# Optimization experiments

Measured on AMD Instinct MI355X. Metric: run time of the kernel, lower is better.

The kernel has to match this reference:

```python
import jax, jax.numpy as jnp
import numpy as np

ATTN_MULT = 8.0
NEG_INF = float('-inf')

N, Q, S, D = 16, 2048, 2048, 64


def setup_inputs() -> dict:
    key = jax.random.key(0)
    kq, kk, kv, kp = jax.random.split(key, 4)
    return {
        "queries_nqd": jax.random.normal(kq, (N, Q, D), dtype=jnp.float32),
        "keys_nsd": jax.random.normal(kk, (N, S, D), dtype=jnp.float32),
        "values_nsv": jax.random.normal(kv, (N, S, D), dtype=jnp.float32),
        "prefix_len_n": jax.random.randint(kp, (N,), 0, S, dtype=jnp.int64 if jax.config.jax_enable_x64 else jnp.int32),
    }


def reference(queries_nqd, keys_nsd, values_nsv, prefix_len_n):
    # attention_type == 'block_diagonal', backend == 'torch', dropout p == 0
    n, q, d = queries_nqd.shape
    s = keys_nsd.shape[1]
    scale = ATTN_MULT / d
    # prefix-block mask: key position < prefix_len (broadcast over queries)
    block_mask_n1s = (jnp.arange(s)[None, None, :] < prefix_len_n[:, None, None])  # [n,1,s]
    diag_mask_qs = jnp.arange(q)[:, None] == jnp.arange(s)[None, :]                # [q,s]
    mask_nqs = block_mask_n1s | diag_mask_qs[None, :, :]                           # [n,q,s]
    scores_nqs = jnp.einsum('nqd,nsd->nqs', queries_nqd, keys_nsd) * scale
    scores_nqs = jnp.where(mask_nqs, scores_nqs, NEG_INF)
    probs_nqs = jax.nn.softmax(scores_nqs, axis=-1)
    return jnp.einsum('nqs,nsv->nqv', probs_nqs, values_nsv)
```

## Files before the change

### kernel.cpp

```cpp
#include <hip/hip_runtime.h>
#include <hip/hip_bf16.h>
#include <math.h>

#define NH 16
#define QL 2048
#define SL 2048
#define DD 64
#define BQ 128
#define NSPLIT 2
#define PSTR 72
#define QK_SCALE_LOG2E 0.1803368801111f

typedef __attribute__((ext_vector_type(8))) short short8;
typedef __attribute__((ext_vector_type(4))) float floatx4;
typedef __attribute__((ext_vector_type(4))) unsigned short ushort4v;
typedef __attribute__((ext_vector_type(8))) unsigned short ushort8v;

__device__ __forceinline__ unsigned short f2bf(float x) {
    unsigned u = __float_as_uint(x);
    u += 0x7FFFu + ((u >> 16) & 1u);
    return (unsigned short)(u >> 16);
}
__device__ __forceinline__ unsigned int f2bf2u(float x, float y) {
    __hip_bfloat162 h = __float22bfloat162_rn(make_float2(x, y));
    return *(unsigned int*)&h;
}
__device__ __forceinline__ float bf2f(unsigned short h) {
    return __uint_as_float((unsigned)h << 16);
}

__device__ __forceinline__ void gld16(const unsigned short* g, unsigned short* l) {
    __builtin_amdgcn_global_load_lds(
        (const __attribute__((address_space(1))) unsigned int*)g,
        (__attribute__((address_space(3))) unsigned int*)l, 16, 0, 0);
}

__global__ __launch_bounds__(512) void k_prep(
    const float* __restrict__ Kf, const float* __restrict__ Vf,
    unsigned short* __restrict__ Kb, unsigned short* __restrict__ Vtb)
{
    __shared__ unsigned short sT[64][PSTR];
    const int bx = (int)blockIdx.x, tid = (int)threadIdx.x;

    const int gidx = bx * 512 + tid;
    #pragma unroll
    for (int k = 0; k < 2; ++k) {
        int idx = gidx + k * (512 * 512);
        float4 v = ((const float4*)Kf)[idx];
        ushort4v h = { f2bf(v.x), f2bf(v.y), f2bf(v.z), f2bf(v.w) };
        *(ushort4v*)(Kb + (size_t)idx * 4) = h;
    }

    const int n = bx >> 5, s0 = (bx & 31) * 64;
    const float* vb = Vf + ((size_t)n * SL + s0) * DD;
    #pragma unroll
    for (int i = 0; i < 2; ++i) {
        int idx = tid + i * 512;
        int r = idx >> 4, c = (idx & 15) << 2;
        float4 v = *(const float4*)(vb + r * DD + c);
        sT[c + 0][r] = f2bf(v.x);
        sT[c + 1][r] = f2bf(v.y);
        sT[c + 2][r] = f2bf(v.z);
        sT[c + 3][r] = f2bf(v.w);
    }
    __syncthreads();
    const int d = tid >> 3, sg = tid & 7;
    unsigned short* out = Vtb + (size_t)n * DD * SL + (size_t)d * SL + s0 + sg * 8;
    ushort8v a;
    #pragma unroll
    for (int i = 0; i < 8; ++i) a[i] = sT[d][sg * 8 + i];
    *(ushort8v*)out = a;
}

__global__ __launch_bounds__(512, 4) void k_attn(
    const float* __restrict__ Qf, const unsigned short* __restrict__ Kb,
    const unsigned short* __restrict__ Vtb, const int* __restrict__ plen_g,
    unsigned short* __restrict__ Opb, float* __restrict__ Lp)
{
    __shared__ unsigned short sK[3][64 * 64];
    __shared__ unsigned short sVt[3][64 * 64];
    __shared__ unsigned short sP[8 * 16 * 64];

    const int flat = (int)blockIdx.x;
    const int sp   = flat >> 8;
    const int rb   = flat & 255;
    const int n    = (rb + sp) & (NH - 1);
    const int qt   = rb >> 4;
    const int q0   = qt * BQ;
    const int plen = plen_g[n];

    const int tid  = (int)threadIdx.x;
    const int wave = tid >> 6, lane = tid & 63, quad = lane >> 4, l16 = lane & 15;

    const int ptiles = (plen + 63) >> 6;
    const int d0     = q0 >> 6;
    const int tdiag  = d0 + sp;
    const int cnt_p  = (ptiles + 1 - sp) >> 1;
    const int total  = cnt_p + (tdiag >= ptiles ? 1 : 0);

    const int qrow  = wave * 16 + l16;
    const int qglob = q0 + qrow;
    const int pmask = (l16 & 7) * 8;

    const unsigned short* kh = Kb  + (size_t)n * SL * DD;
    const unsigned short* vh = Vtb + (size_t)n * DD * SL;

    const int srow = wave * 8 + (lane >> 3);
    const int scol = ((lane & 7) ^ (srow & 7)) * 8;

    auto tile_of = [&](int i) -> int {
        return (i < cnt_p) ? (sp + (i << 1)) : tdiag;
    };
    auto stage = [&](int t, int b) {
        const unsigned short* kg = kh + ((size_t)t << 6) * DD;
        const unsigned short* vg = vh + (t << 6);
        gld16(kg + srow * DD + scol, sK[b] + wave * 512);
        gld16(vg + (size_t)srow * SL + scol, sVt[b] + wave * 512);
    };

    short8 bQ0, bQ1;
    {
        const float* qf = Qf + ((size_t)(n * QL + qglob)) * DD + quad * 8;
        float4 a0 = *(const float4*)(qf);
        float4 a1 = *(const float4*)(qf + 4);
        float4 c0 = *(const float4*)(qf + 32);
        float4 c1 = *(const float4*)(qf + 36);
        const float S = QK_SCALE_LOG2E;
        unsigned int u0[4] = {
            f2bf2u(a0.x * S, a0.y * S), f2bf2u(a0.z * S, a0.w * S),
            f2bf2u(a1.x * S, a1.y * S), f2bf2u(a1.z * S, a1.w * S) };
        unsigned int u1[4] = {
            f2bf2u(c0.x * S, c0.y * S), f2bf2u(c0.z * S, c0.w * S),
            f2bf2u(c1.x * S, c1.y * S), f2bf2u(c1.z * S, c1.w * S) };
        bQ0 = *(short8*)u0;
        bQ1 = *(short8*)u1;
    }

    stage(tile_of(0), 0);
    if (total > 1) stage(tile_of(1), 1);

    floatx4 acc[4];
    #pragma unroll
    for (int dt = 0; dt < 4; ++dt) acc[dt] = (floatx4){0.f, 0.f, 0.f, 0.f};
    float lsum = 0.f;
    unsigned short* pw = sP + qrow * 64;

    int bi = 0;
    int bs = 2;
    for (int i = 0; i < total; ++i) {
        if (i + 2 <= total) {
            asm volatile("s_waitcnt vmcnt(2) lgkmcnt(0)" ::: "memory");
        } else {
            asm volatile("s_waitcnt vmcnt(0) lgkmcnt(0)" ::: "memory");
        }
        __builtin_amdgcn_s_barrier();

        if (i + 2 < total) stage(tile_of(i + 2), bs);

        const unsigned short* sk = sK[bi];
        const unsigned short* sv = sVt[bi];
        const int t  = tile_of(i);
        const int s0 = t << 6;

        floatx4 sf[4];
        #pragma unroll
        for (int st2 = 0; st2 < 4; ++st2) sf[st2] = (floatx4){0.f, 0.f, 0.f, 0.f};
        __builtin_amdgcn_s_setprio(1);
        #pragma unroll
        for (int st2 = 0; st2 < 4; ++st2) {
            int krow = st2 * 16 + l16;
            short8 aK0 = *(const short8*)(sk + krow * 64 + (((0 * 4 + quad) ^ (krow & 7)) * 8));
            short8 aK1 = *(const short8*)(sk + krow * 64 + (((1 * 4 + quad) ^ (krow & 7)) * 8));
            sf[st2] = __builtin_amdgcn_mfma_f32_16x16x32_bf16(aK0, bQ0, sf[st2], 0, 0, 0);
            sf[st2] = __builtin_amdgcn_mfma_f32_16x16x32_bf16(aK1, bQ1, sf[st2], 0, 0, 0);
        }
        __builtin_amdgcn_s_setprio(0);

        if (s0 + 64 <= plen) {
            #pragma unroll
            for (int st2 = 0; st2 < 4; ++st2) {
                float p0 = __builtin_amdgcn_exp2f(sf[st2][0]);
                float p1 = __builtin_amdgcn_exp2f(sf[st2][1]);
                float p2 = __builtin_amdgcn_exp2f(sf[st2][2]);
                float p3 = __builtin_amdgcn_exp2f(sf[st2][3]);
                lsum += (p0 + p1) + (p2 + p3);
                uint2 pk = { f2bf2u(p0, p1), f2bf2u(p2, p3) };
                *(uint2*)(pw + ((st2 * 16 + quad * 4) ^ pmask)) = pk;
            }
        } else {
            #pragma unroll
            for (int st2 = 0; st2 < 4; ++st2) {
                float p[4];
                #pragma unroll
                for (int r2 = 0; r2 < 4; ++r2) {
                    int s = s0 + st2 * 16 + quad * 4 + r2;
                    bool valid = (s < plen) || (s == qglob);
                    p[r2] = __builtin_amdgcn_exp2f(valid ? sf[st2][r2] : -INFINITY);
                    lsum += p[r2];
                }
                uint2 pk = { f2bf2u(p[0], p[1]), f2bf2u(p[2], p[3]) };
                *(uint2*)(pw + ((st2 * 16 + quad * 4) ^ pmask)) = pk;
            }
        }

        __builtin_amdgcn_s_setprio(1);
        #pragma unroll
        for (int ks = 0; ks < 2; ++ks) {
            short8 aP = *(const short8*)(pw + ((ks * 32 + quad * 8) ^ pmask));
            #pragma unroll
            for (int dt = 0; dt < 4; ++dt) {
                int vrow = dt * 16 + l16;
                short8 bV = *(const short8*)(sv + vrow * 64 + (((ks * 4 + quad) ^ (vrow & 7)) * 8));
                acc[dt] = __builtin_amdgcn_mfma_f32_16x16x32_bf16(aP, bV, acc[dt], 0, 0, 0);
            }
        }
        __builtin_amdgcn_s_setprio(0);

        bi = (bi == 2) ? 0 : bi + 1;
        bs = (bs == 2) ? 0 : bs + 1;
    }

    lsum += __shfl_xor(lsum, 16, 64);
    lsum += __shfl_xor(lsum, 32, 64);
    if (quad == 0)
        Lp[((size_t)sp * NH + n) * QL + q0 + qrow] = lsum;

    unsigned short* pws = sP + wave * 16 * 64;
    #pragma unroll
    for (int dt = 0; dt < 4; ++dt) {
        int chunk = dt * 2 + (l16 >> 3);
        #pragma unroll
        for (int r2 = 0; r2 < 4; ++r2) {
            int row = quad * 4 + r2;
            int sw = ((chunk ^ (row & 7)) * 8) + (l16 & 7);
            pws[row * 64 + sw] = f2bf(acc[dt][r2]);
        }
    }
    const size_t qbase = ((size_t)sp * NH + n) * QL + q0 + wave * 16;
    #pragma unroll
    for (int t2 = 0; t2 < 2; ++t2) {
        int row = t2 * 8 + (lane >> 3);
        int chunk = lane & 7;
        int sw = (chunk ^ (row & 7)) * 8;
        ushort8v val = *(const ushort8v*)(pws + row * 64 + sw);
        *(ushort8v*)(Opb + (qbase + row) * DD + chunk * 8) = val;
    }
}

__global__ __launch_bounds__(512) void k_combine(
    const unsigned short* __restrict__ Opb, const float* __restrict__ Lp,
    float* __restrict__ Og)
{
    const int idx = (int)(blockIdx.x * 512 + threadIdx.x);
    const int d8 = idx & 7;
    const int q  = (idx >> 3) & (QL - 1);
    const int n  = idx >> 14;
    float s[8];
    #pragma unroll
    for (int j = 0; j < 8; ++j) s[j] = 0.f;
    float l = 0.f;
    #pragma unroll
    for (int sp = 0; sp < NSPLIT; ++sp) {
        const unsigned short* ob = Opb + (((size_t)sp * NH + n) * QL + q) * DD + d8 * 8;
        ushort8v v = *(const ushort8v*)ob;
        #pragma unroll
        for (int j = 0; j < 8; ++j) s[j] += bf2f(v[j]);
        l += Lp[((size_t)sp * NH + n) * QL + q];
    }
    const float inv = 1.0f / l;
    float4 o0 = { s[0] * inv, s[1] * inv, s[2] * inv, s[3] * inv };
    float4 o1 = { s[4] * inv, s[5] * inv, s[6] * inv, s[7] * inv };
    float* og = Og + ((size_t)n * QL + q) * DD + d8 * 8;
    *(float4*)og = o0;
    *(float4*)(og + 4) = o1;
}

extern "C" void kernel_launch(void* const* d_in, const int* in_sizes, int n_in,
                              void* d_out, int out_size, void* d_ws, size_t ws_size,
                              hipStream_t stream) {
    const float* Qf   = (const float*)d_in[0];
    const float* Kf   = (const float*)d_in[1];
    const float* Vf   = (const float*)d_in[2];
    const int*   plen = (const int*)d_in[3];
    float* Og = (float*)d_out;

    char* ws = (char*)d_ws;
    unsigned short* Kb  = (unsigned short*)(ws);
    unsigned short* Vtb = (unsigned short*)(ws + (4u << 20));
    unsigned short* Opb = (unsigned short*)(ws + (8u << 20));
    float*          Lp  = (float*)(ws + (16u << 20));

    k_prep<<<512, 512, 0, stream>>>(Kf, Vf, Kb, Vtb);
    k_attn<<<NSPLIT * 256, 512, 0, stream>>>(Qf, Kb, Vtb, plen, Opb, Lp);
    k_combine<<<512, 512, 0, stream>>>(Opb, Lp, Og);
}
```

Measured before the change: 104.4 us.

## Fuse split-KV combine into attention kernel using two wave groups per block

The two KV splits, previously separate blocks, now run as two 512-thread groups inside one 1024-thread block that share a block barrier. The partial outputs and row sums are merged through shared memory and the normalized fp32 result is written directly. This removes the combine kernel launch and the global round trip of bf16 partials and row sums. In exchange it doubles the shared memory per block. Both groups must loop to the larger tile count because they share a barrier, and the block size limits how many blocks fit per CU.

```diff
diff --git a/kernel.cpp b/kernel.cpp
--- a/kernel.cpp
+++ b/kernel.cpp
@@ -7,7 +7,6 @@
 #define SL 2048
 #define DD 64
 #define BQ 128
-#define NSPLIT 2
 #define PSTR 72
 #define QK_SCALE_LOG2E 0.1803368801111f
 
@@ -72,31 +71,35 @@
     *(ushort8v*)out = a;
 }
 
-__global__ __launch_bounds__(512, 4) void k_attn(
+__global__ __launch_bounds__(1024, 4) void k_attn(
     const float* __restrict__ Qf, const unsigned short* __restrict__ Kb,
     const unsigned short* __restrict__ Vtb, const int* __restrict__ plen_g,
-    unsigned short* __restrict__ Opb, float* __restrict__ Lp)
+    float* __restrict__ Og)
 {
-    __shared__ unsigned short sK[3][64 * 64];
-    __shared__ unsigned short sVt[3][64 * 64];
-    __shared__ unsigned short sP[8 * 16 * 64];
-
-    const int flat = (int)blockIdx.x;
-    const int sp   = flat >> 8;
-    const int rb   = flat & 255;
-    const int n    = (rb + sp) & (NH - 1);
-    const int qt   = rb >> 4;
+    __shared__ unsigned short sK[2][3][64 * 64];
+    __shared__ unsigned short sVt[2][3][64 * 64];
+    __shared__ unsigned short sP[2][8 * 16 * 64];
+    __shared__ float lsh[2][128];
+
+    const int bx   = (int)blockIdx.x;
+    const int n    = bx >> 4;
+    const int qt   = bx & 15;
     const int q0   = qt * BQ;
     const int plen = plen_g[n];
 
     const int tid  = (int)threadIdx.x;
-    const int wave = tid >> 6, lane = tid & 63, quad = lane >> 4, l16 = lane & 15;
+    const int g    = tid >> 9;
+    const int wave = (tid >> 6) & 7;
+    const int lane = tid & 63, quad = lane >> 4, l16 = lane & 15;
 
     const int ptiles = (plen + 63) >> 6;
     const int d0     = q0 >> 6;
-    const int tdiag  = d0 + sp;
-    const int cnt_p  = (ptiles + 1 - sp) >> 1;
-    const int total  = cnt_p + (tdiag >= ptiles ? 1 : 0);
+    const int tot0   = ((ptiles + 1) >> 1) + (d0 >= ptiles ? 1 : 0);
+    const int tot1   = (ptiles >> 1) + (d0 + 1 >= ptiles ? 1 : 0);
+    const int mtotal = (tot0 > tot1) ? tot0 : tot1;
+    const int cnt_p  = g ? (ptiles >> 1) : ((ptiles + 1) >> 1);
+    const int total  = g ? tot1 : tot0;
+    const int tdiag  = d0 + g;
 
     const int qrow  = wave * 16 + l16;
     const int qglob = q0 + qrow;
@@ -109,13 +112,13 @@
     const int scol = ((lane & 7) ^ (srow & 7)) * 8;
 
     auto tile_of = [&](int i) -> int {
-        return (i < cnt_p) ? (sp + (i << 1)) : tdiag;
+        return (i < cnt_p) ? (g + (i << 1)) : tdiag;
     };
     auto stage = [&](int t, int b) {
         const unsigned short* kg = kh + ((size_t)t << 6) * DD;
         const unsigned short* vg = vh + (t << 6);
-        gld16(kg + srow * DD + scol, sK[b] + wave * 512);
-        gld16(vg + (size_t)srow * SL + scol, sVt[b] + wave * 512);
+        gld16(kg + srow * DD + scol, sK[g][b] + wave * 512);
+        gld16(vg + (size_t)srow * SL + scol, sVt[g][b] + wave * 512);
     };
 
     short8 bQ0, bQ1;
@@ -143,78 +146,83 @@
     #pragma unroll
     for (int dt = 0; dt < 4; ++dt) acc[dt] = (floatx4){0.f, 0.f, 0.f, 0.f};
     float lsum = 0.f;
-    unsigned short* pw = sP + qrow * 64;
+    unsigned short* pw = sP[g] + qrow * 64;
 
     int bi = 0;
     int bs = 2;
-    for (int i = 0; i < total; ++i) {
-        if (i + 2 <= total) {
-            asm volatile("s_waitcnt vmcnt(2) lgkmcnt(0)" ::: "memory");
-        } else {
-            asm volatile("s_waitcnt vmcnt(0) lgkmcnt(0)" ::: "memory");
+    for (int i = 0; i < mtotal; ++i) {
+        if (i < total) {
+            if (i + 2 <= total) {
+                asm volatile("s_waitcnt vmcnt(2) lgkmcnt(0)" ::: "memory");
+            } else {
+                asm volatile("s_waitcnt vmcnt(0) lgkmcnt(0)" ::: "memory");
+            }
         }
         __builtin_amdgcn_s_barrier();
-
-        if (i + 2 < total) stage(tile_of(i + 2), bs);
-
-        const unsigned short* sk = sK[bi];
-        const unsigned short* sv = sVt[bi];
-        const int t  = tile_of(i);
-        const int s0 = t << 6;
-
-        floatx4 sf[4];
-        #pragma unroll
-        for (int st2 = 0; st2 < 4; ++st2) sf[st2] = (floatx4){0.f, 0.f, 0.f, 0.f};
-        __builtin_amdgcn_s_setprio(1);
-        #pragma unroll
-        for (int st2 = 0; st2 < 4; ++st2) {
-            int krow = st2 * 16 + l16;
-            short8 aK0 = *(const short8*)(sk + krow * 64 + (((0 * 4 + quad) ^ (krow & 7)) * 8));
-            short8 aK1 = *(const short8*)(sk + krow * 64 + (((1 * 4 + quad) ^ (krow & 7)) * 8));
-            sf[st2] = __builtin_amdgcn_mfma_f32_16x16x32_bf16(aK0, bQ0, sf[st2], 0, 0, 0);
-            sf[st2] = __builtin_amdgcn_mfma_f32_16x16x32_bf16(aK1, bQ1, sf[st2], 0, 0, 0);
-        }
-        __builtin_amdgcn_s_setprio(0);
-
-        if (s0 + 64 <= plen) {
+        __builtin_amdgcn_sched_barrier(0);
+
+        if (i < total) {
+            if (i + 2 < total) stage(tile_of(i + 2), bs);
+
+            const unsigned short* sk = sK[g][bi];
+            const unsigned short* sv = sVt[g][bi];
+            const int t  = tile_of(i);
+            const int s0 = t << 6;
+
+            floatx4 sf[4];
+            #pragma unroll
+            for (int st2 = 0; st2 < 4; ++st2) sf[st2] = (floatx4){0.f, 0.f, 0.f, 0.f};
+            __builtin_amdgcn_s_setprio(1);
             #pragma unroll
             for (int st2 = 0; st2 < 4; ++st2) {
-                float p0 = __builtin_amdgcn_exp2f(sf[st2][0]);
-                float p1 = __builtin_amdgcn_exp2f(sf[st2][1]);
-                float p2 = __builtin_amdgcn_exp2f(sf[st2][2]);
-                float p3 = __builtin_amdgcn_exp2f(sf[st2][3]);
-                lsum += (p0 + p1) + (p2 + p3);
-                uint2 pk = { f2bf2u(p0, p1), f2bf2u(p2, p3) };
-                *(uint2*)(pw + ((st2 * 16 + quad * 4) ^ pmask)) = pk;
-            }
-        } else {
-            #pragma unroll
-            for (int st2 = 0; st2 < 4; ++st2) {
-                float p[4];
+                int krow = st2 * 16 + l16;
+                short8 aK0 = *(const short8*)(sk + krow * 64 + (((0 * 4 + quad) ^ (krow & 7)) * 8));
+                short8 aK1 = *(const short8*)(sk + krow * 64 + (((1 * 4 + quad) ^ (krow & 7)) * 8));
+                sf[st2] = __builtin_amdgcn_mfma_f32_16x16x32_bf16(aK0, bQ0, sf[st2], 0, 0, 0);
+                sf[st2] = __builtin_amdgcn_mfma_f32_16x16x32_bf16(aK1, bQ1, sf[st2], 0, 0, 0);
+            }
+            __builtin_amdgcn_s_setprio(0);
+
+            if (s0 + 64 <= plen) {
                 #pragma unroll
-                for (int r2 = 0; r2 < 4; ++r2) {
-                    int s = s0 + st2 * 16 + quad * 4 + r2;
-                    bool valid = (s < plen) || (s == qglob);
-                    p[r2] = __builtin_amdgcn_exp2f(valid ? sf[st2][r2] : -INFINITY);
-                    lsum += p[r2];
+                for (int st2 = 0; st2 < 4; ++st2) {
+                    float p0 = __builtin_amdgcn_exp2f(sf[st2][0]);
+                    float p1 = __builtin_amdgcn_exp2f(sf[st2][1]);
+                    float p2 = __builtin_amdgcn_exp2f(sf[st2][2]);
+                    float p3 = __builtin_amdgcn_exp2f(sf[st2][3]);
+                    lsum += (p0 + p1) + (p2 + p3);
+                    uint2 pk = { f2bf2u(p0, p1), f2bf2u(p2, p3) };
+                    *(uint2*)(pw + ((st2 * 16 + quad * 4) ^ pmask)) = pk;
                 }
-                uint2 pk = { f2bf2u(p[0], p[1]), f2bf2u(p[2], p[3]) };
-                *(uint2*)(pw + ((st2 * 16 + quad * 4) ^ pmask)) = pk;
-            }
-        }
-
-        __builtin_amdgcn_s_setprio(1);
-        #pragma unroll
-        for (int ks = 0; ks < 2; ++ks) {
-            short8 aP = *(const short8*)(pw + ((ks * 32 + quad * 8) ^ pmask));
-            #pragma unroll
-            for (int dt = 0; dt < 4; ++dt) {
-                int vrow = dt * 16 + l16;
-                short8 bV = *(const short8*)(sv + vrow * 64 + (((ks * 4 + quad) ^ (vrow & 7)) * 8));
-                acc[dt] = __builtin_amdgcn_mfma_f32_16x16x32_bf16(aP, bV, acc[dt], 0, 0, 0);
-            }
-        }
-        __builtin_amdgcn_s_setprio(0);
+            } else {
+                #pragma unroll
+                for (int st2 = 0; st2 < 4; ++st2) {
+                    float p[4];
+                    #pragma unroll
+                    for (int r2 = 0; r2 < 4; ++r2) {
+                        int s = s0 + st2 * 16 + quad * 4 + r2;
+                        bool valid = (s < plen) || (s == qglob);
+                        p[r2] = __builtin_amdgcn_exp2f(valid ? sf[st2][r2] : -INFINITY);
+                        lsum += p[r2];
+                    }
+                    uint2 pk = { f2bf2u(p[0], p[1]), f2bf2u(p[2], p[3]) };
+                    *(uint2*)(pw + ((st2 * 16 + quad * 4) ^ pmask)) = pk;
+                }
+            }
+
+            __builtin_amdgcn_s_setprio(1);
+            #pragma unroll
+            for (int ks = 0; ks < 2; ++ks) {
+                short8 aP = *(const short8*)(pw + ((ks * 32 + quad * 8) ^ pmask));
+                #pragma unroll
+                for (int dt = 0; dt < 4; ++dt) {
+                    int vrow = dt * 16 + l16;
+                    short8 bV = *(const short8*)(sv + vrow * 64 + (((ks * 4 + quad) ^ (vrow & 7)) * 8));
+                    acc[dt] = __builtin_amdgcn_mfma_f32_16x16x32_bf16(aP, bV, acc[dt], 0, 0, 0);
+                }
+            }
+            __builtin_amdgcn_s_setprio(0);
+        }
 
         bi = (bi == 2) ? 0 : bi + 1;
         bs = (bs == 2) ? 0 : bs + 1;
@@ -223,56 +231,45 @@
     lsum += __shfl_xor(lsum, 16, 64);
     lsum += __shfl_xor(lsum, 32, 64);
     if (quad == 0)
-        Lp[((size_t)sp * NH + n) * QL + q0 + qrow] = lsum;
-
-    unsigned short* pws = sP + wave * 16 * 64;
-    #pragma unroll
-    for (int dt = 0; dt < 4; ++dt) {
-        int chunk = dt * 2 + (l16 >> 3);
+        lsh[g][wave * 16 + l16] = lsum;
+
+    if (g == 1) {
+        unsigned short* pws = sP[1] + wave * 16 * 64;
+        #pragma unroll
+        for (int dt = 0; dt < 4; ++dt) {
+            int chunk = dt * 2 + (l16 >> 3);
+            #pragma unroll
+            for (int r2 = 0; r2 < 4; ++r2) {
+                int row = quad * 4 + r2;
+                int sw = ((chunk ^ (row & 7)) * 8) + (l16 & 7);
+                pws[row * 64 + sw] = f2bf(acc[dt][r2]);
+            }
+        }
+    }
+    __syncthreads();
+
+    if (g == 0) {
+        const unsigned short* pws = sP[1] + wave * 16 * 64;
+        float inv[4];
         #pragma unroll
         for (int r2 = 0; r2 < 4; ++r2) {
             int row = quad * 4 + r2;
-            int sw = ((chunk ^ (row & 7)) * 8) + (l16 & 7);
-            pws[row * 64 + sw] = f2bf(acc[dt][r2]);
-        }
-    }
-    const size_t qbase = ((size_t)sp * NH + n) * QL + q0 + wave * 16;
-    #pragma unroll
-    for (int t2 = 0; t2 < 2; ++t2) {
-        int row = t2 * 8 + (lane >> 3);
-        int chunk = lane & 7;
-        int sw = (chunk ^ (row & 7)) * 8;
-        ushort8v val = *(const ushort8v*)(pws + row * 64 + sw);
-        *(ushort8v*)(Opb + (qbase + row) * DD + chunk * 8) = val;
-    }
-}
-
-__global__ __launch_bounds__(512) void k_combine(
-    const unsigned short* __restrict__ Opb, const float* __restrict__ Lp,
-    float* __restrict__ Og)
-{
-    const int idx = (int)(blockIdx.x * 512 + threadIdx.x);
-    const int d8 = idx & 7;
-    const int q  = (idx >> 3) & (QL - 1);
-    const int n  = idx >> 14;
-    float s[8];
-    #pragma unroll
-    for (int j = 0; j < 8; ++j) s[j] = 0.f;
-    float l = 0.f;
-    #pragma unroll
-    for (int sp = 0; sp < NSPLIT; ++sp) {
-        const unsigned short* ob = Opb + (((size_t)sp * NH + n) * QL + q) * DD + d8 * 8;
-        ushort8v v = *(const ushort8v*)ob;
+            float lt = lsh[0][wave * 16 + row] + lsh[1][wave * 16 + row];
+            inv[r2] = 1.0f / lt;
+        }
+        float* ob = Og + ((size_t)n * QL + q0 + wave * 16) * DD;
         #pragma unroll
-        for (int j = 0; j < 8; ++j) s[j] += bf2f(v[j]);
-        l += Lp[((size_t)sp * NH + n) * QL + q];
-    }
-    const float inv = 1.0f / l;
-    float4 o0 = { s[0] * inv, s[1] * inv, s[2] * inv, s[3] * inv };
-    float4 o1 = { s[4] * inv, s[5] * inv, s[6] * inv, s[7] * inv };
-    float* og = Og + ((size_t)n * QL + q) * DD + d8 * 8;
-    *(float4*)og = o0;
-    *(float4*)(og + 4) = o1;
+        for (int dt = 0; dt < 4; ++dt) {
+            int chunk = dt * 2 + (l16 >> 3);
+            #pragma unroll
+            for (int r2 = 0; r2 < 4; ++r2) {
+                int row = quad * 4 + r2;
+                int sw = ((chunk ^ (row & 7)) * 8) + (l16 & 7);
+                float o = (acc[dt][r2] + bf2f(pws[row * 64 + sw])) * inv[r2];
+                ob[row * DD + dt * 16 + l16] = o;
+            }
+        }
+    }
 }
 
 extern "C" void kernel_launch(void* const* d_in, const int* in_sizes, int n_in,
@@ -287,10 +284,7 @@
     char* ws = (char*)d_ws;
     unsigned short* Kb  = (unsigned short*)(ws);
     unsigned short* Vtb = (unsigned short*)(ws + (4u << 20));
-    unsigned short* Opb = (unsigned short*)(ws + (8u << 20));
-    float*          Lp  = (float*)(ws + (16u << 20));
 
     k_prep<<<512, 512, 0, stream>>>(Kf, Vf, Kb, Vtb);
-    k_attn<<<NSPLIT * 256, 512, 0, stream>>>(Qf, Kb, Vtb, plen, Opb, Lp);
-    k_combine<<<512, 512, 0, stream>>>(Opb, Lp, Og);
-}
+    k_attn<<<NH * (QL / BQ), 1024, 0, stream>>>(Qf, Kb, Vtb, plen, Og);
+}
```

New measurement: 106.1 us. About the same (+1.7%).

## Process two query halves per block to reuse K/V tiles, split keys four ways

Applied to the files above, without the earlier changes.

Each attention block now covers 256 query rows as two 128-row halves sharing every staged K and V^T tile, so the LDS loads and global staging are amortised over twice the MFMA work. To keep the grid at 512 blocks, the key dimension is split four ways instead of two, which doubles the partial-output traffic read by the combine kernel. Q is converted and pre-scaled to bf16 in the prep kernel rather than inside the attention kernel. The doubled accumulators and score registers raise register pressure under the existing launch bound, which risks spills or lower occupancy.

```diff
diff --git a/kernel.cpp b/kernel.cpp
--- a/kernel.cpp
+++ b/kernel.cpp
@@ -6,8 +6,8 @@
 #define QL 2048
 #define SL 2048
 #define DD 64
-#define BQ 128
-#define NSPLIT 2
+#define BQ 256
+#define NSPLIT 4
 #define PSTR 72
 #define QK_SCALE_LOG2E 0.1803368801111f
 
@@ -36,19 +36,27 @@
 }
 
 __global__ __launch_bounds__(512) void k_prep(
-    const float* __restrict__ Kf, const float* __restrict__ Vf,
-    unsigned short* __restrict__ Kb, unsigned short* __restrict__ Vtb)
+    const float* __restrict__ Qf, const float* __restrict__ Kf, const float* __restrict__ Vf,
+    unsigned short* __restrict__ Qb, unsigned short* __restrict__ Kb, unsigned short* __restrict__ Vtb)
 {
     __shared__ unsigned short sT[64][PSTR];
     const int bx = (int)blockIdx.x, tid = (int)threadIdx.x;
-
     const int gidx = bx * 512 + tid;
+
     #pragma unroll
     for (int k = 0; k < 2; ++k) {
         int idx = gidx + k * (512 * 512);
         float4 v = ((const float4*)Kf)[idx];
         ushort4v h = { f2bf(v.x), f2bf(v.y), f2bf(v.z), f2bf(v.w) };
         *(ushort4v*)(Kb + (size_t)idx * 4) = h;
+    }
+    #pragma unroll
+    for (int k = 0; k < 2; ++k) {
+        int idx = gidx + k * (512 * 512);
+        float4 v = ((const float4*)Qf)[idx];
+        const float S = QK_SCALE_LOG2E;
+        ushort4v h = { f2bf(v.x * S), f2bf(v.y * S), f2bf(v.z * S), f2bf(v.w * S) };
+        *(ushort4v*)(Qb + (size_t)idx * 4) = h;
     }
 
     const int n = bx >> 5, s0 = (bx & 31) * 64;
@@ -73,17 +81,17 @@
 }
 
 __global__ __launch_bounds__(512, 4) void k_attn(
-    const float* __restrict__ Qf, const unsigned short* __restrict__ Kb,
+    const unsigned short* __restrict__ Qb, const unsigned short* __restrict__ Kb,
     const unsigned short* __restrict__ Vtb, const int* __restrict__ plen_g,
     unsigned short* __restrict__ Opb, float* __restrict__ Lp)
 {
     __shared__ unsigned short sK[3][64 * 64];
     __shared__ unsigned short sVt[3][64 * 64];
-    __shared__ unsigned short sP[8 * 16 * 64];
+    __shared__ unsigned short sP[2][8 * 16 * 64];
 
     const int flat = (int)blockIdx.x;
-    const int sp   = flat >> 8;
-    const int rb   = flat & 255;
+    const int sp   = flat >> 7;
+    const int rb   = flat & 127;
     const int n    = (rb + sp) & (NH - 1);
     const int qt   = rb >> 4;
     const int q0   = qt * BQ;
@@ -95,11 +103,12 @@
     const int ptiles = (plen + 63) >> 6;
     const int d0     = q0 >> 6;
     const int tdiag  = d0 + sp;
-    const int cnt_p  = (ptiles + 1 - sp) >> 1;
+    const int cnt_p  = (ptiles + 3 - sp) >> 2;
     const int total  = cnt_p + (tdiag >= ptiles ? 1 : 0);
 
     const int qrow  = wave * 16 + l16;
-    const int qglob = q0 + qrow;
+    const int qgA   = q0 + qrow;
+    const int qgB   = qgA + 128;
     const int pmask = (l16 & 7) * 8;
 
     const unsigned short* kh = Kb  + (size_t)n * SL * DD;
@@ -109,7 +118,7 @@
     const int scol = ((lane & 7) ^ (srow & 7)) * 8;
 
     auto tile_of = [&](int i) -> int {
-        return (i < cnt_p) ? (sp + (i << 1)) : tdiag;
+        return (i < cnt_p) ? (sp + (i << 2)) : tdiag;
     };
     auto stage = [&](int t, int b) {
         const unsigned short* kg = kh + ((size_t)t << 6) * DD;
@@ -118,32 +127,25 @@
         gld16(vg + (size_t)srow * SL + scol, sVt[b] + wave * 512);
     };
 
-    short8 bQ0, bQ1;
-    {
-        const float* qf = Qf + ((size_t)(n * QL + qglob)) * DD + quad * 8;
-        float4 a0 = *(const float4*)(qf);
-        float4 a1 = *(const float4*)(qf + 4);
-        float4 c0 = *(const float4*)(qf + 32);
-        float4 c1 = *(const float4*)(qf + 36);
-        const float S = QK_SCALE_LOG2E;
-        unsigned int u0[4] = {
-            f2bf2u(a0.x * S, a0.y * S), f2bf2u(a0.z * S, a0.w * S),
-            f2bf2u(a1.x * S, a1.y * S), f2bf2u(a1.z * S, a1.w * S) };
-        unsigned int u1[4] = {
-            f2bf2u(c0.x * S, c0.y * S), f2bf2u(c0.z * S, c0.w * S),
-            f2bf2u(c1.x * S, c1.y * S), f2bf2u(c1.z * S, c1.w * S) };
-        bQ0 = *(short8*)u0;
-        bQ1 = *(short8*)u1;
-    }
+    const unsigned short* qbA = Qb + ((size_t)n * QL + qgA) * DD;
+    const unsigned short* qbB = qbA + 128 * DD;
+    short8 bQ0A = *(const short8*)(qbA + quad * 8);
+    short8 bQ1A = *(const short8*)(qbA + 32 + quad * 8);
+    short8 bQ0B = *(const short8*)(qbB + quad * 8);
+    short8 bQ1B = *(const short8*)(qbB + 32 + quad * 8);
 
     stage(tile_of(0), 0);
     if (total > 1) stage(tile_of(1), 1);
 
-    floatx4 acc[4];
-    #pragma unroll
-    for (int dt = 0; dt < 4; ++dt) acc[dt] = (floatx4){0.f, 0.f, 0.f, 0.f};
-    float lsum = 0.f;
-    unsigned short* pw = sP + qrow * 64;
+    floatx4 accA[4], accB[4];
+    #pragma unroll
+    for (int dt = 0; dt < 4; ++dt) {
+        accA[dt] = (floatx4){0.f, 0.f, 0.f, 0.f};
+        accB[dt] = (floatx4){0.f, 0.f, 0.f, 0.f};
+    }
+    float lsumA = 0.f, lsumB = 0.f;
+    unsigned short* pwA = sP[0] + qrow * 64;
+    unsigned short* pwB = sP[1] + qrow * 64;
 
     int bi = 0;
     int bs = 2;
@@ -162,56 +164,75 @@
         const int t  = tile_of(i);
         const int s0 = t << 6;
 
-        floatx4 sf[4];
-        #pragma unroll
-        for (int st2 = 0; st2 < 4; ++st2) sf[st2] = (floatx4){0.f, 0.f, 0.f, 0.f};
+        floatx4 sfA[4], sfB[4];
+        #pragma unroll
+        for (int st2 = 0; st2 < 4; ++st2) {
+            sfA[st2] = (floatx4){0.f, 0.f, 0.f, 0.f};
+            sfB[st2] = (floatx4){0.f, 0.f, 0.f, 0.f};
+        }
         __builtin_amdgcn_s_setprio(1);
         #pragma unroll
         for (int st2 = 0; st2 < 4; ++st2) {
             int krow = st2 * 16 + l16;
             short8 aK0 = *(const short8*)(sk + krow * 64 + (((0 * 4 + quad) ^ (krow & 7)) * 8));
             short8 aK1 = *(const short8*)(sk + krow * 64 + (((1 * 4 + quad) ^ (krow & 7)) * 8));
-            sf[st2] = __builtin_amdgcn_mfma_f32_16x16x32_bf16(aK0, bQ0, sf[st2], 0, 0, 0);
-            sf[st2] = __builtin_amdgcn_mfma_f32_16x16x32_bf16(aK1, bQ1, sf[st2], 0, 0, 0);
+            sfA[st2] = __builtin_amdgcn_mfma_f32_16x16x32_bf16(aK0, bQ0A, sfA[st2], 0, 0, 0);
+            sfA[st2] = __builtin_amdgcn_mfma_f32_16x16x32_bf16(aK1, bQ1A, sfA[st2], 0, 0, 0);
+            sfB[st2] = __builtin_amdgcn_mfma_f32_16x16x32_bf16(aK0, bQ0B, sfB[st2], 0, 0, 0);
+            sfB[st2] = __builtin_amdgcn_mfma_f32_16x16x32_bf16(aK1, bQ1B, sfB[st2], 0, 0, 0);
         }
         __builtin_amdgcn_s_setprio(0);
 
         if (s0 + 64 <= plen) {
             #pragma unroll
             for (int st2 = 0; st2 < 4; ++st2) {
-                float p0 = __builtin_amdgcn_exp2f(sf[st2][0]);
-                float p1 = __builtin_amdgcn_exp2f(sf[st2][1]);
-                float p2 = __builtin_amdgcn_exp2f(sf[st2][2]);
-                float p3 = __builtin_amdgcn_exp2f(sf[st2][3]);
-                lsum += (p0 + p1) + (p2 + p3);
-                uint2 pk = { f2bf2u(p0, p1), f2bf2u(p2, p3) };
-                *(uint2*)(pw + ((st2 * 16 + quad * 4) ^ pmask)) = pk;
+                float a0 = __builtin_amdgcn_exp2f(sfA[st2][0]);
+                float a1 = __builtin_amdgcn_exp2f(sfA[st2][1]);
+                float a2 = __builtin_amdgcn_exp2f(sfA[st2][2]);
+                float a3 = __builtin_amdgcn_exp2f(sfA[st2][3]);
+                lsumA += (a0 + a1) + (a2 + a3);
+                uint2 pkA = { f2bf2u(a0, a1), f2bf2u(a2, a3) };
+                *(uint2*)(pwA + ((st2 * 16 + quad * 4) ^ pmask)) = pkA;
+                float b0 = __builtin_amdgcn_exp2f(sfB[st2][0]);
+                float b1 = __builtin_amdgcn_exp2f(sfB[st2][1]);
+                float b2 = __builtin_amdgcn_exp2f(sfB[st2][2]);
+                float b3 = __builtin_amdgcn_exp2f(sfB[st2][3]);
+                lsumB += (b0 + b1) + (b2 + b3);
+                uint2 pkB = { f2bf2u(b0, b1), f2bf2u(b2, b3) };
+                *(uint2*)(pwB + ((st2 * 16 + quad * 4) ^ pmask)) = pkB;
             }
         } else {
             #pragma unroll
             for (int st2 = 0; st2 < 4; ++st2) {
-                float p[4];
+                float pa[4], pb[4];
                 #pragma unroll
                 for (int r2 = 0; r2 < 4; ++r2) {
                     int s = s0 + st2 * 16 + quad * 4 + r2;
-                    bool valid = (s < plen) || (s == qglob);
-                    p[r2] = __builtin_amdgcn_exp2f(valid ? sf[st2][r2] : -INFINITY);
-                    lsum += p[r2];
+                    bool va = (s < plen) || (s == qgA);
+                    bool vb = (s < plen) || (s == qgB);
+                    pa[r2] = __builtin_amdgcn_exp2f(va ? sfA[st2][r2] : -INFINITY);
+                    pb[r2] = __builtin_amdgcn_exp2f(vb ? sfB[st2][r2] : -INFINITY);
+                    lsumA += pa[r2];
+                    lsumB += pb[r2];
                 }
-                uint2 pk = { f2bf2u(p[0], p[1]), f2bf2u(p[2], p[3]) };
-                *(uint2*)(pw + ((st2 * 16 + quad * 4) ^ pmask)) = pk;
+                uint2 pkA = { f2bf2u(pa[0], pa[1]), f2bf2u(pa[2], pa[3]) };
+                uint2 pkB = { f2bf2u(pb[0], pb[1]), f2bf2u(pb[2], pb[3]) };
+                *(uint2*)(pwA + ((st2 * 16 + quad * 4) ^ pmask)) = pkA;
+                *(uint2*)(pwB + ((st2 * 16 + quad * 4) ^ pmask)) = pkB;
             }
         }
 
         __builtin_amdgcn_s_setprio(1);
         #pragma unroll
         for (int ks = 0; ks < 2; ++ks) {
-            short8 aP = *(const short8*)(pw + ((ks * 32 + quad * 8) ^ pmask));
+            short8 aPA = *(const short8*)(pwA + ((ks * 32 + quad * 8) ^ pmask));
+            short8 aPB = *(const short8*)(pwB + ((ks * 32 + quad * 8) ^ pmask));
             #pragma unroll
             for (int dt = 0; dt < 4; ++dt) {
                 int vrow = dt * 16 + l16;
                 short8 bV = *(const short8*)(sv + vrow * 64 + (((ks * 4 + quad) ^ (vrow & 7)) * 8));
-                acc[dt] = __builtin_amdgcn_mfma_f32_16x16x32_bf16(aP, bV, acc[dt], 0, 0, 0);
+                accA[dt] = __builtin_amdgcn_mfma_f32_16x16x32_bf16(aPA, bV, accA[dt], 0, 0, 0);
+                accB[dt] = __builtin_amdgcn_mfma_f32_16x16x32_bf16(aPB, bV, accB[dt], 0, 0, 0);
             }
         }
         __builtin_amdgcn_s_setprio(0);
@@ -220,12 +241,17 @@
         bs = (bs == 2) ? 0 : bs + 1;
     }
 
-    lsum += __shfl_xor(lsum, 16, 64);
-    lsum += __shfl_xor(lsum, 32, 64);
-    if (quad == 0)
-        Lp[((size_t)sp * NH + n) * QL + q0 + qrow] = lsum;
-
-    unsigned short* pws = sP + wave * 16 * 64;
+    lsumA += __shfl_xor(lsumA, 16, 64);
+    lsumA += __shfl_xor(lsumA, 32, 64);
+    lsumB += __shfl_xor(lsumB, 16, 64);
+    lsumB += __shfl_xor(lsumB, 32, 64);
+    if (quad == 0) {
+        Lp[((size_t)sp * NH + n) * QL + qgA] = lsumA;
+        Lp[((size_t)sp * NH + n) * QL + qgB] = lsumB;
+    }
+
+    unsigned short* pwsA = sP[0] + wave * 16 * 64;
+    unsigned short* pwsB = sP[1] + wave * 16 * 64;
     #pragma unroll
     for (int dt = 0; dt < 4; ++dt) {
         int chunk = dt * 2 + (l16 >> 3);
@@ -233,17 +259,21 @@
         for (int r2 = 0; r2 < 4; ++r2) {
             int row = quad * 4 + r2;
             int sw = ((chunk ^ (row & 7)) * 8) + (l16 & 7);
-            pws[row * 64 + sw] = f2bf(acc[dt][r2]);
-        }
-    }
-    const size_t qbase = ((size_t)sp * NH + n) * QL + q0 + wave * 16;
+            pwsA[row * 64 + sw] = f2bf(accA[dt][r2]);
+            pwsB[row * 64 + sw] = f2bf(accB[dt][r2]);
+        }
+    }
+    const size_t qbaseA = ((size_t)sp * NH + n) * QL + q0 + wave * 16;
+    const size_t qbaseB = qbaseA + 128;
     #pragma unroll
     for (int t2 = 0; t2 < 2; ++t2) {
         int row = t2 * 8 + (lane >> 3);
         int chunk = lane & 7;
         int sw = (chunk ^ (row & 7)) * 8;
-        ushort8v val = *(const ushort8v*)(pws + row * 64 + sw);
-        *(ushort8v*)(Opb + (qbase + row) * DD + chunk * 8) = val;
+        ushort8v valA = *(const ushort8v*)(pwsA + row * 64 + sw);
+        ushort8v valB = *(const ushort8v*)(pwsB + row * 64 + sw);
+        *(ushort8v*)(Opb + (qbaseA + row) * DD + chunk * 8) = valA;
+        *(ushort8v*)(Opb + (qbaseB + row) * DD + chunk * 8) = valB;
     }
 }
 
@@ -287,10 +317,11 @@
     char* ws = (char*)d_ws;
     unsigned short* Kb  = (unsigned short*)(ws);
     unsigned short* Vtb = (unsigned short*)(ws + (4u << 20));
-    unsigned short* Opb = (unsigned short*)(ws + (8u << 20));
-    float*          Lp  = (float*)(ws + (16u << 20));
-
-    k_prep<<<512, 512, 0, stream>>>(Kf, Vf, Kb, Vtb);
-    k_attn<<<NSPLIT * 256, 512, 0, stream>>>(Qf, Kb, Vtb, plen, Opb, Lp);
+    unsigned short* Qb  = (unsigned short*)(ws + (8u << 20));
+    unsigned short* Opb = (unsigned short*)(ws + (12u << 20));
+    float*          Lp  = (float*)(ws + (28u << 20));
+
+    k_prep<<<512, 512, 0, stream>>>(Qf, Kf, Vf, Qb, Kb, Vtb);
+    k_attn<<<NSPLIT * 128, 512, 0, stream>>>(Qb, Kb, Vtb, plen, Opb, Lp);
     k_combine<<<512, 512, 0, stream>>>(Opb, Lp, Og);
 }
```

Result: slower. 117.3 us (+12.4%).

## Fuse split-KV combine into attention kernel via last-block atomic counter

Applied to the files above, without the earlier changes.

Removes the separate combine kernel launch. Each attention block bumps a per-(head, q-tile) atomic counter after writing its partial output, and the last of the two splits reduces both partials into the final fp32 output. The counter is zeroed in the prep kernel. This saves one kernel launch and its scheduling gap, at the cost of a threadfence, an atomic per block, and tail work on the last-arriving block.

```diff
diff --git a/kernel.cpp b/kernel.cpp
--- a/kernel.cpp
+++ b/kernel.cpp
@@ -37,10 +37,14 @@
 
 __global__ __launch_bounds__(512) void k_prep(
     const float* __restrict__ Kf, const float* __restrict__ Vf,
-    unsigned short* __restrict__ Kb, unsigned short* __restrict__ Vtb)
+    unsigned short* __restrict__ Kb, unsigned short* __restrict__ Vtb,
+    int* __restrict__ cnt)
 {
     __shared__ unsigned short sT[64][PSTR];
     const int bx = (int)blockIdx.x, tid = (int)threadIdx.x;
+
+    if (bx == 0 && tid < NH * (QL / BQ))
+        cnt[tid] = 0;
 
     const int gidx = bx * 512 + tid;
     #pragma unroll
@@ -75,11 +79,13 @@
 __global__ __launch_bounds__(512, 4) void k_attn(
     const float* __restrict__ Qf, const unsigned short* __restrict__ Kb,
     const unsigned short* __restrict__ Vtb, const int* __restrict__ plen_g,
-    unsigned short* __restrict__ Opb, float* __restrict__ Lp)
+    unsigned short* __restrict__ Opb, float* __restrict__ Lp,
+    int* __restrict__ cnt, float* __restrict__ Og)
 {
     __shared__ unsigned short sK[3][64 * 64];
     __shared__ unsigned short sVt[3][64 * 64];
     __shared__ unsigned short sP[8 * 16 * 64];
+    __shared__ int last;
 
     const int flat = (int)blockIdx.x;
     const int sp   = flat >> 8;
@@ -245,34 +251,46 @@
         ushort8v val = *(const ushort8v*)(pws + row * 64 + sw);
         *(ushort8v*)(Opb + (qbase + row) * DD + chunk * 8) = val;
     }
-}
-
-__global__ __launch_bounds__(512) void k_combine(
-    const unsigned short* __restrict__ Opb, const float* __restrict__ Lp,
-    float* __restrict__ Og)
-{
-    const int idx = (int)(blockIdx.x * 512 + threadIdx.x);
-    const int d8 = idx & 7;
-    const int q  = (idx >> 3) & (QL - 1);
-    const int n  = idx >> 14;
-    float s[8];
-    #pragma unroll
-    for (int j = 0; j < 8; ++j) s[j] = 0.f;
-    float l = 0.f;
-    #pragma unroll
-    for (int sp = 0; sp < NSPLIT; ++sp) {
-        const unsigned short* ob = Opb + (((size_t)sp * NH + n) * QL + q) * DD + d8 * 8;
-        ushort8v v = *(const ushort8v*)ob;
-        #pragma unroll
-        for (int j = 0; j < 8; ++j) s[j] += bf2f(v[j]);
-        l += Lp[((size_t)sp * NH + n) * QL + q];
-    }
+
+    __threadfence();
+    __syncthreads();
+    if (tid == 0) {
+        int old = __hip_atomic_fetch_add(&cnt[n * 16 + qt], 1,
+                                         __ATOMIC_ACQ_REL, __HIP_MEMORY_SCOPE_AGENT);
+        last = (old == NSPLIT - 1);
+    }
+    __syncthreads();
+    if (!last) return;
+    __threadfence();
+
+    const int tq = tid >> 2;
+    const int dq = (tid & 3) << 4;
+    const int q  = q0 + tq;
+    float l = Lp[((size_t)0 * NH + n) * QL + q] + Lp[((size_t)1 * NH + n) * QL + q];
     const float inv = 1.0f / l;
-    float4 o0 = { s[0] * inv, s[1] * inv, s[2] * inv, s[3] * inv };
-    float4 o1 = { s[4] * inv, s[5] * inv, s[6] * inv, s[7] * inv };
-    float* og = Og + ((size_t)n * QL + q) * DD + d8 * 8;
-    *(float4*)og = o0;
-    *(float4*)(og + 4) = o1;
+    float o[16];
+    #pragma unroll
+    for (int sp2 = 0; sp2 < NSPLIT; ++sp2) {
+        const unsigned short* ob = Opb + (((size_t)sp2 * NH + n) * QL + q) * DD + dq;
+        ushort8v v0 = *(const ushort8v*)(ob);
+        ushort8v v1 = *(const ushort8v*)(ob + 8);
+        if (sp2 == 0) {
+            #pragma unroll
+            for (int j = 0; j < 8; ++j) { o[j] = bf2f(v0[j]); o[8 + j] = bf2f(v1[j]); }
+        } else {
+            #pragma unroll
+            for (int j = 0; j < 8; ++j) { o[j] += bf2f(v0[j]); o[8 + j] += bf2f(v1[j]); }
+        }
+    }
+    float* og = Og + ((size_t)n * QL + q) * DD + dq;
+    float4 f0 = { o[0] * inv,  o[1] * inv,  o[2] * inv,  o[3] * inv };
+    float4 f1 = { o[4] * inv,  o[5] * inv,  o[6] * inv,  o[7] * inv };
+    float4 f2 = { o[8] * inv,  o[9] * inv,  o[10] * inv, o[11] * inv };
+    float4 f3 = { o[12] * inv, o[13] * inv, o[14] * inv, o[15] * inv };
+    *(float4*)(og)      = f0;
+    *(float4*)(og + 4)  = f1;
+    *(float4*)(og + 8)  = f2;
+    *(float4*)(og + 12) = f3;
 }
 
 extern "C" void kernel_launch(void* const* d_in, const int* in_sizes, int n_in,
@@ -289,8 +307,8 @@
     unsigned short* Vtb = (unsigned short*)(ws + (4u << 20));
     unsigned short* Opb = (unsigned short*)(ws + (8u << 20));
     float*          Lp  = (float*)(ws + (16u << 20));
-
-    k_prep<<<512, 512, 0, stream>>>(Kf, Vf, Kb, Vtb);
-    k_attn<<<NSPLIT * 256, 512, 0, stream>>>(Qf, Kb, Vtb, plen, Opb, Lp);
-    k_combine<<<512, 512, 0, stream>>>(Opb, Lp, Og);
-}
+    int*            cnt = (int*)(ws + (17u << 20));
+
+    k_prep<<<512, 512, 0, stream>>>(Kf, Vf, Kb, Vtb, cnt);
+    k_attn<<<NSPLIT * 256, 512, 0, stream>>>(Qf, Kb, Vtb, plen, Opb, Lp, cnt, Og);
+}
```

Result: slower. 316.8 us (+203.5%).
